# Optimization experiments

Measured on AMD Instinct MI355X. Metric: run time of the kernel, lower is better.

## Reference

```python
import jax, jax.numpy as jnp
import numpy as np

IGNORE_LABEL = -1
W_F = 1.0
EPS = 1e-7


def setup_inputs() -> dict:
    key = jax.random.key(0)
    k1, k2 = jax.random.split(key)
    B, H, W = 16, 1024, 1024
    o_f = jax.random.uniform(k1, (B, 3, H, W), dtype=jnp.float32)
    target = jax.random.randint(k2, (B, H, W), 0, 20).astype(jnp.int64)
    return {"o_f": o_f, "target": target}


def reference(o_f, target):
    # o_f: [B, 3, h, w]  (channels 0,1 = spatial offsets, channel 2 = confidence f)
    # target: [B, h, w] int labels
    B = o_f.shape[0]
    h, w = target.shape[1], target.shape[2]

    # coordinate grid (xm along width, ym along height), same as torch.linspace(0, w-1, w)
    xm = jnp.arange(w, dtype=o_f.dtype)  # [w]
    ym = jnp.arange(h, dtype=o_f.dtype)  # [h]

    # spatial_pix = offsets + grid, then floor + clamp -> integer gather coords
    x = jnp.floor(o_f[:, 0] + xm[None, None, :]).astype(jnp.int32)  # [B,h,w]
    y = jnp.floor(o_f[:, 1] + ym[None, :, None]).astype(jnp.int32)  # [B,h,w]
    x = jnp.clip(x, 0, w - 1)
    y = jnp.clip(y, 0, h - 1)

    # tmp_target[tmp_target == ignore_label] = 0
    tmp_target = jnp.where(target == IGNORE_LABEL, 0, target)  # [B,h,w]

    # H_seed = tmp_target[b, y, x] (per-batch coordinate gather), vectorized via flat indices
    flat_idx = (y * w + x).reshape(B, -1)  # [B, h*w]
    H_s = jnp.take_along_axis(tmp_target.reshape(B, -1), flat_idx.astype(jnp.int64), axis=1)
    H_s = H_s.reshape(B, h, w)

    mask = tmp_target == H_s  # [B,h,w] bool; mask2 = ~mask
    f = o_f[:, 2]  # [B,h,w]

    # sum(-log(f+eps)) over mask + sum(-log(1-f+eps)) over ~mask, per batch, / (h*w)
    per_pix = jnp.where(mask, -jnp.log(f + EPS), -jnp.log(1.0 - f + EPS))
    f_loss = jnp.sum(per_pix, axis=(1, 2)) / (h * w)  # [B]
    return W_F * jnp.mean(f_loss)
```

## Files before the change

### kernel.cpp

```cpp
#include <hip/hip_runtime.h>
#include <math.h>

constexpr int Wd = 1024;
constexpr int Hd = 1024;
constexpr int HW = Wd * Hd;
constexpr int NPIX = 16 * HW;
constexpr int NGRP = NPIX / 4;
constexpr float EPSF = 1e-7f;
constexpr float INV_TOTAL = 1.0f / 16777216.0f;

constexpr int NBLK = 2048;
constexpr int NTHR = 256;
constexpr int NITER = NGRP / (NBLK * NTHR);

__global__ __launch_bounds__(256) void conf_loss_partial(
    const float* __restrict__ of,
    const int*   __restrict__ tgt,
    float*       __restrict__ partial)
{
    const float4* of4 = (const float4*)of;
    const int4*   t4  = (const int4*)tgt;
    const int gid0 = blockIdx.x * NTHR + threadIdx.x;

    float sum = 0.0f;
#pragma unroll
    for (int it = 0; it < NITER; ++it) {
        const int g   = gid0 + it * (NBLK * NTHR);
        const int p0  = g << 2;
        const int b   = p0 >> 20;
        const int rem = p0 & (HW - 1);
        const int i   = rem >> 10;
        const int j   = rem & (Wd - 1);

        const int baseU = b * 3 * HW + rem;
        const float4 u0 = of4[(baseU          ) >> 2];
        const float4 u1 = of4[(baseU +     HW ) >> 2];
        const float4 fv = of4[(baseU + 2 * HW ) >> 2];
        const int4   tv = t4[(b * HW + rem) >> 2];

        const float fi = (float)i;
        const float us[4] = {u0.x, u0.y, u0.z, u0.w};
        const float vs[4] = {u1.x, u1.y, u1.z, u1.w};
        const float fs[4] = {fv.x, fv.y, fv.z, fv.w};
        const int   ts[4] = {tv.x, tv.y, tv.z, tv.w};

#pragma unroll
        for (int k = 0; k < 4; ++k) {
            int x = (int)floorf(us[k] + (float)(j + k));
            int y = (int)floorf(vs[k] + fi);
            x = min(max(x, 0), Wd - 1);
            y = min(max(y, 0), Hd - 1);
            int t = ts[k];
            t = (t == -1) ? 0 : t;
            int hs = tgt[b * HW + y * Wd + x];
            hs = (hs == -1) ? 0 : hs;
            const float val = (t == hs) ? (fs[k] + EPSF) : (1.0f - fs[k] + EPSF);
            sum -= __logf(val);
        }
    }

#pragma unroll
    for (int off = 32; off > 0; off >>= 1)
        sum += __shfl_down(sum, off, 64);

    __shared__ float lsum[4];
    const int lane = threadIdx.x & 63;
    const int wv   = threadIdx.x >> 6;
    if (lane == 0) lsum[wv] = sum;
    __syncthreads();
    if (threadIdx.x == 0)
        partial[blockIdx.x] = lsum[0] + lsum[1] + lsum[2] + lsum[3];
}

__global__ __launch_bounds__(256) void conf_loss_final(
    const float* __restrict__ partial, float* __restrict__ out)
{
    float s = 0.0f;
#pragma unroll
    for (int it = 0; it < NBLK / NTHR; ++it)
        s += partial[it * NTHR + threadIdx.x];

#pragma unroll
    for (int off = 32; off > 0; off >>= 1)
        s += __shfl_down(s, off, 64);

    __shared__ float lsum[4];
    const int lane = threadIdx.x & 63;
    const int wv   = threadIdx.x >> 6;
    if (lane == 0) lsum[wv] = s;
    __syncthreads();
    if (threadIdx.x == 0)
        out[0] = (lsum[0] + lsum[1] + lsum[2] + lsum[3]) * INV_TOTAL;
}

extern "C" void kernel_launch(void* const* d_in, const int* in_sizes, int n_in,
                              void* d_out, int out_size, void* d_ws, size_t ws_size,
                              hipStream_t stream) {
    const float* of  = (const float*)d_in[0];
    const int*   tgt = (const int*)d_in[1];
    float*       out = (float*)d_out;
    float*       partial = (float*)d_ws;

    conf_loss_partial<<<NBLK, NTHR, 0, stream>>>(of, tgt, partial);
    conf_loss_final<<<1, NTHR, 0, stream>>>(partial, out);
}
```

Before: 314.7 us.

## Add fast path skipping target loads when offsets map each pixel to itself

Each pixel first checks whether its floored offset coordinates land back on the pixel itself. In that case the gathered label trivially equals the pixel's own label, so the loss is just -log(f+eps) and neither the target tensor nor the gather is read. Pixels that fail the check fall back to the full gather path, which replaces the speculative term with the correct one. This cuts memory traffic when offsets are small, at the cost of re-reading the inputs for any pixels that miss the check.

```diff
diff --git a/kernel.cpp b/kernel.cpp
--- a/kernel.cpp
+++ b/kernel.cpp
@@ -19,43 +19,72 @@
     float*       __restrict__ partial)
 {
     const float4* of4 = (const float4*)of;
-    const int4*   t4  = (const int4*)tgt;
     const int gid0 = blockIdx.x * NTHR + threadIdx.x;
 
+    const int p0  = gid0 << 2;
+    const int b0  = p0 >> 20;
+    const int rem = p0 & (HW - 1);
+    const int i   = rem >> 10;
+    const int j   = rem & (Wd - 1);
+    const float fi = (float)i;
+    const float fj0 = (float)j;
+
     float sum = 0.0f;
+    int bad = 0;
+
 #pragma unroll
     for (int it = 0; it < NITER; ++it) {
-        const int g   = gid0 + it * (NBLK * NTHR);
-        const int p0  = g << 2;
-        const int b   = p0 >> 20;
-        const int rem = p0 & (HW - 1);
-        const int i   = rem >> 10;
-        const int j   = rem & (Wd - 1);
-
+        const int b = b0 + 2 * it;
         const int baseU = b * 3 * HW + rem;
         const float4 u0 = of4[(baseU          ) >> 2];
         const float4 u1 = of4[(baseU +     HW ) >> 2];
         const float4 fv = of4[(baseU + 2 * HW ) >> 2];
-        const int4   tv = t4[(b * HW + rem) >> 2];
 
-        const float fi = (float)i;
-        const float us[4] = {u0.x, u0.y, u0.z, u0.w};
-        const float vs[4] = {u1.x, u1.y, u1.z, u1.w};
-        const float fs[4] = {fv.x, fv.y, fv.z, fv.w};
-        const int   ts[4] = {tv.x, tv.y, tv.z, tv.w};
+        bool ok =
+            (floorf(u0.x + fj0)        == fj0)        &
+            (floorf(u0.y + fj0 + 1.0f) == fj0 + 1.0f) &
+            (floorf(u0.z + fj0 + 2.0f) == fj0 + 2.0f) &
+            (floorf(u0.w + fj0 + 3.0f) == fj0 + 3.0f) &
+            (floorf(u1.x + fi) == fi) & (floorf(u1.y + fi) == fi) &
+            (floorf(u1.z + fi) == fi) & (floorf(u1.w + fi) == fi);
+        bad |= (ok ? 0 : 1) << it;
 
+        sum -= __logf(fv.x + EPSF) + __logf(fv.y + EPSF) +
+               __logf(fv.z + EPSF) + __logf(fv.w + EPSF);
+    }
+
+    if (__any(bad != 0)) {
+        if (bad) {
 #pragma unroll
-        for (int k = 0; k < 4; ++k) {
-            int x = (int)floorf(us[k] + (float)(j + k));
-            int y = (int)floorf(vs[k] + fi);
-            x = min(max(x, 0), Wd - 1);
-            y = min(max(y, 0), Hd - 1);
-            int t = ts[k];
-            t = (t == -1) ? 0 : t;
-            int hs = tgt[b * HW + y * Wd + x];
-            hs = (hs == -1) ? 0 : hs;
-            const float val = (t == hs) ? (fs[k] + EPSF) : (1.0f - fs[k] + EPSF);
-            sum -= __logf(val);
+            for (int it = 0; it < NITER; ++it) {
+                if ((bad >> it) & 1) {
+                    const int b = b0 + 2 * it;
+                    const int baseU = b * 3 * HW + rem;
+                    const float4 u0 = of4[(baseU          ) >> 2];
+                    const float4 u1 = of4[(baseU +     HW ) >> 2];
+                    const float4 fv = of4[(baseU + 2 * HW ) >> 2];
+                    const int4  tv = ((const int4*)tgt)[(b * HW + rem) >> 2];
+                    const float us[4] = {u0.x, u0.y, u0.z, u0.w};
+                    const float vs[4] = {u1.x, u1.y, u1.z, u1.w};
+                    const float fs[4] = {fv.x, fv.y, fv.z, fv.w};
+                    const int   ts[4] = {tv.x, tv.y, tv.z, tv.w};
+#pragma unroll
+                    for (int k = 0; k < 4; ++k) {
+                        int x = (int)floorf(us[k] + (float)(j + k));
+                        int y = (int)floorf(vs[k] + fi);
+                        x = min(max(x, 0), Wd - 1);
+                        y = min(max(y, 0), Hd - 1);
+                        int t = ts[k];
+                        t = (t == -1) ? 0 : t;
+                        int hs = tgt[b * HW + y * Wd + x];
+                        hs = (hs == -1) ? 0 : hs;
+                        if (t != hs) {
+                            sum += __logf(fs[k] + EPSF)
+                                 - __logf(1.0f - fs[k] + EPSF);
+                        }
+                    }
+                }
+            }
         }
     }
 
```

Measured after the change: 300.0 us. 1.05x faster.

## Skip target gathers when offsets map each pixel back to itself

Applied to the files above, without the earlier changes.

Each block now handles 8 full rows of one image, and all offset and confidence loads are issued up front. For each group of 4 pixels it checks whether floor(offset+coord) lands on the pixel itself. In that case the label comparison is trivially true, so only -log(f+eps) is accumulated and neither the target nor the gathered label is read. A wave-level fallback reads labels and applies the correction only for pixels whose gather coordinate differs. This cuts target traffic and random gathers when offsets are small, which the uniform [0,1) inputs make the common case, at the cost of divergence and more registers.

```diff
diff --git a/kernel.cpp b/kernel.cpp
--- a/kernel.cpp
+++ b/kernel.cpp
@@ -4,65 +4,80 @@
 constexpr int Wd = 1024;
 constexpr int Hd = 1024;
 constexpr int HW = Wd * Hd;
-constexpr int NPIX = 16 * HW;
-constexpr int NGRP = NPIX / 4;
 constexpr float EPSF = 1e-7f;
 constexpr float INV_TOTAL = 1.0f / 16777216.0f;
 
-constexpr int NBLK = 2048;
 constexpr int NTHR = 256;
-constexpr int NITER = NGRP / (NBLK * NTHR);
+constexpr int BPB  = 128;
+constexpr int NBLK = 16 * BPB;
+constexpr int NIT  = 8;
 
 __global__ __launch_bounds__(256) void conf_loss_partial(
     const float* __restrict__ of,
     const int*   __restrict__ tgt,
     float*       __restrict__ partial)
 {
-    const float4* of4 = (const float4*)of;
-    const int4*   t4  = (const int4*)tgt;
-    const int gid0 = blockIdx.x * NTHR + threadIdx.x;
+    const int b    = blockIdx.x >> 7;
+    const int blk  = blockIdx.x & (BPB - 1);
+    const int j    = threadIdx.x << 2;
+    const int row0 = blk << 3;
+    const int base = b * 3 * HW + row0 * Wd + j;
 
+    const float4* pu = (const float4*)(of + base);
+    const float4* pv = (const float4*)(of + base + HW);
+    const float4* pf = (const float4*)(of + base + 2 * HW);
+
+    float4 U[NIT], V[NIT], F[NIT];
+#pragma unroll
+    for (int it = 0; it < NIT; ++it) {
+        U[it] = pu[it * (Wd / 4)];
+        V[it] = pv[it * (Wd / 4)];
+        F[it] = pf[it * (Wd / 4)];
+    }
+
+    const float fj = (float)j;
     float sum = 0.0f;
 #pragma unroll
-    for (int it = 0; it < NITER; ++it) {
-        const int g   = gid0 + it * (NBLK * NTHR);
-        const int p0  = g << 2;
-        const int b   = p0 >> 20;
-        const int rem = p0 & (HW - 1);
-        const int i   = rem >> 10;
-        const int j   = rem & (Wd - 1);
+    for (int it = 0; it < NIT; ++it) {
+        const int   i  = row0 + it;
+        const float fi = (float)i;
 
-        const int baseU = b * 3 * HW + rem;
-        const float4 u0 = of4[(baseU          ) >> 2];
-        const float4 u1 = of4[(baseU +     HW ) >> 2];
-        const float4 fv = of4[(baseU + 2 * HW ) >> 2];
-        const int4   tv = t4[(b * HW + rem) >> 2];
+        sum -= __logf(F[it].x + EPSF) + __logf(F[it].y + EPSF) +
+               __logf(F[it].z + EPSF) + __logf(F[it].w + EPSF);
 
-        const float fi = (float)i;
-        const float us[4] = {u0.x, u0.y, u0.z, u0.w};
-        const float vs[4] = {u1.x, u1.y, u1.z, u1.w};
-        const float fs[4] = {fv.x, fv.y, fv.z, fv.w};
-        const int   ts[4] = {tv.x, tv.y, tv.z, tv.w};
+        const bool ok =
+            (floorf(U[it].x + fj)        == fj)        &
+            (floorf(U[it].y + fj + 1.0f) == fj + 1.0f) &
+            (floorf(U[it].z + fj + 2.0f) == fj + 2.0f) &
+            (floorf(U[it].w + fj + 3.0f) == fj + 3.0f) &
+            (floorf(V[it].x + fi) == fi) & (floorf(V[it].y + fi) == fi) &
+            (floorf(V[it].z + fi) == fi) & (floorf(V[it].w + fi) == fi);
 
+        if (__any(!ok)) {
+            const float us[4] = {U[it].x, U[it].y, U[it].z, U[it].w};
+            const float vs[4] = {V[it].x, V[it].y, V[it].z, V[it].w};
+            const float fs[4] = {F[it].x, F[it].y, F[it].z, F[it].w};
+            const int pixbase = b * HW + i * Wd + j;
 #pragma unroll
-        for (int k = 0; k < 4; ++k) {
-            int x = (int)floorf(us[k] + (float)(j + k));
-            int y = (int)floorf(vs[k] + fi);
-            x = min(max(x, 0), Wd - 1);
-            y = min(max(y, 0), Hd - 1);
-            int t = ts[k];
-            t = (t == -1) ? 0 : t;
-            int hs = tgt[b * HW + y * Wd + x];
-            hs = (hs == -1) ? 0 : hs;
-            const float val = (t == hs) ? (fs[k] + EPSF) : (1.0f - fs[k] + EPSF);
-            sum -= __logf(val);
+            for (int k = 0; k < 4; ++k) {
+                int x = (int)floorf(us[k] + (float)(j + k));
+                int y = (int)floorf(vs[k] + fi);
+                if (x != j + k || y != i) {
+                    x = min(max(x, 0), Wd - 1);
+                    y = min(max(y, 0), Hd - 1);
+                    int t = tgt[pixbase + k];          t  = (t  == -1) ? 0 : t;
+                    int hs = tgt[b * HW + y * Wd + x]; hs = (hs == -1) ? 0 : hs;
+                    if (t != hs)
+                        sum += __logf(fs[k] + EPSF)
+                             - __logf(1.0f - fs[k] + EPSF);
+                }
+            }
         }
     }
 
 #pragma unroll
     for (int off = 32; off > 0; off >>= 1)
         sum += __shfl_down(sum, off, 64);
-
     __shared__ float lsum[4];
     const int lane = threadIdx.x & 63;
     const int wv   = threadIdx.x >> 6;
@@ -79,11 +94,9 @@
 #pragma unroll
     for (int it = 0; it < NBLK / NTHR; ++it)
         s += partial[it * NTHR + threadIdx.x];
-
 #pragma unroll
     for (int off = 32; off > 0; off >>= 1)
         s += __shfl_down(s, off, 64);
-
     __shared__ float lsum[4];
     const int lane = threadIdx.x & 63;
     const int wv   = threadIdx.x >> 6;
```

Measured after the change: 298.3 us. 5.2% less time.
